# Kernel optimization log

Hardware: AMD Instinct MI355X
Metric: run time of the kernel (lower is better)

## Reference

```python
import jax, jax.numpy as jnp
import numpy as np

B, L, D, H = 4, 2048, 1024, 16
HD = D // H  # head dim = 64


def setup_inputs() -> dict:
    key = jax.random.key(0)
    ks = jax.random.split(key, 8)
    std_qkv = np.sqrt(D + D // H).astype(np.float32)  # matches nn.init.normal_ std in source
    xav = np.sqrt(2.0 / (D + D)).astype(np.float32)   # xavier_normal_ for fc_out
    return {
        "query": jax.random.normal(ks[0], (B, L, D), dtype=jnp.float32),
        "key": jax.random.normal(ks[1], (B, L, D), dtype=jnp.float32),
        "value": jax.random.normal(ks[2], (B, L, D), dtype=jnp.float32),
        "Wq": jax.random.normal(ks[3], (D, D), dtype=jnp.float32) * std_qkv,
        "Wk": jax.random.normal(ks[4], (D, D), dtype=jnp.float32) * std_qkv,
        "Wv": jax.random.normal(ks[5], (D, D), dtype=jnp.float32) * std_qkv,
        "Wo": jax.random.normal(ks[6], (D, D), dtype=jnp.float32) * xav,
        "bo": jnp.zeros((D,), dtype=jnp.float32),
    }


def reference(query, key, value, Wq, Wk, Wv, Wo, bo):
    # Linear projections (torch Linear: x @ W.T), then split heads: b l (h k) -> b h l k
    def split_heads(x):
        b, l, _ = x.shape
        return x.reshape(b, l, H, HD).transpose(0, 2, 1, 3)

    q = split_heads(query @ Wq.T)   # [B,H,L,HD]
    k = split_heads(key @ Wk.T)     # [B,H,T,HD]
    v = split_heads(value @ Wv.T)   # [B,H,T,HD]

    scale = 1.0 / np.sqrt(HD).astype(np.float32)
    energy = jnp.einsum("bhlk,bhtk->bhlt", q, k) * scale  # [B,H,L,T]
    attention = jax.nn.softmax(energy, axis=3)
    out = jnp.einsum("bhlt,bhtv->bhlv", attention, v)     # [B,H,L,HD]
    # b h l v -> b l (h v)
    out = out.transpose(0, 2, 1, 3).reshape(B, L, D)
    out = out @ Wo.T + bo  # dropout_rate=0.0 -> identity
    return out, attention
```

## Files before the change

kernel.cpp:

```cpp
#include <hip/hip_runtime.h>
#include <math.h>

#define Bb 4
#define Ls 2048
#define Dd 1024
#define Hh 16
#define HDm 64
#define ML (Bb*Ls)

typedef double f64x4 __attribute__((ext_vector_type(4)));
typedef float  f32x4 __attribute__((ext_vector_type(4)));
typedef short  bf16x8 __attribute__((ext_vector_type(8)));
typedef unsigned int u32;
typedef unsigned short u16;

__device__ __forceinline__ void gload16(const void* g, void* l) {
  __builtin_amdgcn_global_load_lds(
      (const __attribute__((address_space(1))) u32*)g,
      (__attribute__((address_space(3))) u32*)l, 16, 0, 0);
}

__device__ __forceinline__ u16 f2bf(float f) {
  u32 u = __float_as_uint(f);
  u += 0x7FFFu + ((u >> 16) & 1u);
  return (u16)(u >> 16);
}

__global__ __launch_bounds__(256) void f32_to_bf16(
    const float* __restrict__ in, u16* __restrict__ out, int n8) {
  int i = blockIdx.x * 256 + threadIdx.x;
  if (i >= n8) return;
  const float4* p = (const float4*)(in + (size_t)i * 8);
  float4 a = p[0], c = p[1];
  union { u16 h[8]; uint4 v; } o;
  o.h[0] = f2bf(a.x); o.h[1] = f2bf(a.y); o.h[2] = f2bf(a.z); o.h[3] = f2bf(a.w);
  o.h[4] = f2bf(c.x); o.h[5] = f2bf(c.y); o.h[6] = f2bf(c.z); o.h[7] = f2bf(c.w);
  *(uint4*)(out + (size_t)i * 8) = o.v;
}

__device__ __forceinline__ void gemm_core_nt(
    const float* __restrict__ A, const float* __restrict__ B,
    int bm, int bn, int w, int lrow, int lk, f64x4 acc[4]) {
  const int K = Dd;
  __shared__ __align__(16) float As[2][64 * 16];
  __shared__ __align__(16) float Bs[2][64 * 16];
  const int tid = threadIdx.x;
  const int r = tid >> 2, blk = tid & 3;
  const int sblk = blk ^ ((r >> 1) & 3);
  const int sxw = ((lrow >> 1) & 3) << 2;
  const float* ga = A + (size_t)(bm + r) * K + 4 * sblk;
  const float* gb = B + (size_t)(bn + r) * K + 4 * sblk;

#pragma unroll
  for (int j = 0; j < 4; j++) acc[j] = (f64x4){0., 0., 0., 0.};

  char* la0 = (char*)&As[0][0] + w * 1024;
  char* lb0 = (char*)&Bs[0][0] + w * 1024;
  char* la1 = (char*)&As[1][0] + w * 1024;
  char* lb1 = (char*)&Bs[1][0] + w * 1024;

  gload16(ga, la0);
  gload16(gb, lb0);
  __syncthreads();

  int cur = 0;
  for (int k0 = 16; k0 <= K; k0 += 16) {
    if (k0 < K) {
      gload16(ga + k0, cur ? la0 : la1);
      gload16(gb + k0, cur ? lb0 : lb1);
    }
    const float* Abuf = &As[cur][0];
    const float* Bbuf = &Bs[cur][0];
#pragma unroll
    for (int t = 0; t < 4; t++) {
      double a = (double)Abuf[(16 * w + lrow) * 16 + ((4 * t + lk) ^ sxw)];
#pragma unroll
      for (int j = 0; j < 4; j++) {
        double bv = (double)Bbuf[(16 * j + lrow) * 16 + ((4 * t + lk) ^ sxw)];
        acc[j] = __builtin_amdgcn_mfma_f64_16x16x4f64(a, bv, acc[j], 0, 0, 0);
      }
    }
    __syncthreads();
    cur ^= 1;
  }
}

__global__ __launch_bounds__(256) void gemm_nt_mfma_f64(
    const float* __restrict__ A, const float* __restrict__ B,
    double* __restrict__ C, double outscale) {
  const int tid = threadIdx.x;
  const int lane = tid & 63;
  const int w = tid >> 6;
  const int lrow = lane & 15, lk = lane >> 4;
  const int bm = blockIdx.y * 64, bn = blockIdx.x * 64;
  f64x4 acc[4];
  gemm_core_nt(A, B, bm, bn, w, lrow, lk, acc);
#pragma unroll
  for (int j = 0; j < 4; j++)
#pragma unroll
    for (int d = 0; d < 4; d++) {
      size_t m = (size_t)(bm + 16 * w + 4 * d + lk);
      C[m * Dd + bn + 16 * j + lrow] = acc[j][d] * outscale;
    }
}

__global__ __launch_bounds__(256) void gemm_nt_bf16(
    const u16* __restrict__ A, const u16* __restrict__ B,
    const float* __restrict__ bias, u16* __restrict__ Cb,
    float* __restrict__ Cf) {
  const int K = Dd;
  __shared__ __align__(16) u16 Asb[2][64 * 32];
  __shared__ __align__(16) u16 Bsb[2][64 * 32];
  const int tid = threadIdx.x;
  const int lane = tid & 63;
  const int w = tid >> 6;
  const int lrow = lane & 15, lk = lane >> 4;
  const int bm = blockIdx.y * 64, bn = blockIdx.x * 64;

  const int srow = 16 * w + (lane >> 2);
  const u16* ga = A + (size_t)(bm + srow) * K + 8 * (lane & 3);
  const u16* gb = B + (size_t)(bn + srow) * K + 8 * (lane & 3);
  char* la0 = (char*)&Asb[0][0] + w * 1024;
  char* lb0 = (char*)&Bsb[0][0] + w * 1024;
  char* la1 = (char*)&Asb[1][0] + w * 1024;
  char* lb1 = (char*)&Bsb[1][0] + w * 1024;

  f32x4 acc[4] = {{0.f,0.f,0.f,0.f},{0.f,0.f,0.f,0.f},
                  {0.f,0.f,0.f,0.f},{0.f,0.f,0.f,0.f}};

  gload16(ga, la0);
  gload16(gb, lb0);
  __syncthreads();

  int cur = 0;
  for (int k0 = 32; k0 <= K; k0 += 32) {
    if (k0 < K) {
      gload16(ga + k0, cur ? la0 : la1);
      gload16(gb + k0, cur ? lb0 : lb1);
    }
    const u16* Ab = &Asb[cur][0];
    const u16* Bt = &Bsb[cur][0];
    bf16x8 afr = *(const bf16x8*)&Ab[(16 * w + lrow) * 32 + 8 * lk];
#pragma unroll
    for (int j = 0; j < 4; j++) {
      bf16x8 bfr = *(const bf16x8*)&Bt[(16 * j + lrow) * 32 + 8 * lk];
      acc[j] = __builtin_amdgcn_mfma_f32_16x16x32_bf16(afr, bfr, acc[j], 0, 0, 0);
    }
    __syncthreads();
    cur ^= 1;
  }

#pragma unroll
  for (int j = 0; j < 4; j++)
#pragma unroll
    for (int r = 0; r < 4; r++) {
      size_t m = (size_t)(bm + 16 * w + 4 * lk + r);
      int n = bn + 16 * j + lrow;
      float v = acc[j][r];
      if (bias) v += bias[n];
      if (Cf) Cf[m * Dd + n] = v;
      else    Cb[m * Dd + n] = f2bf(v);
    }
}

__global__ __launch_bounds__(256) void attn_flash(
    double* __restrict__ Qd, const double* __restrict__ Kd,
    const u16* __restrict__ Vf, float* __restrict__ attn,
    u16* __restrict__ O) {
  __shared__ __align__(16) double Kbuf[2][32 * 64];
  __shared__ __align__(16) u16    Vb16[2][32 * 64];
  __shared__ __align__(16) u16    Pb[4][16 * 32];
  __shared__ __align__(16) float  Fs[4][16];

  const int tid = threadIdx.x;
  const int lane = tid & 63;
  const int w = tid >> 6;
  const int lrow = lane & 15;
  const int lk = lane >> 4;
  const int blk = blockIdx.x;
  const int qt = blk & 31;
  const int h = (blk >> 5) & 15;
  const int b = blk >> 9;
  const int l0 = qt * 64;

  const double* Qg = Qd + ((size_t)(b * Ls + l0)) * Dd + h * HDm;
  const double* Kg = Kd + ((size_t)b * Ls) * Dd + h * HDm;
  const u16*    Vg = Vf + ((size_t)b * Ls) * Dd + h * HDm;
  float* aout = attn + ((size_t)((b * Hh + h) * Ls + l0)) * Ls;

  double qreg[16];
#pragma unroll
  for (int t = 0; t < 16; t++)
    qreg[t] = Qg[(size_t)(16 * w + lrow) * Dd + 4 * t + lk];

  const int l16 = (lane & 31) * 16;
  const int halfk = lane >> 5;
  const int sx = (lrow & 7) << 1;

  auto stage = [&](int kts, int bsel) {
#pragma unroll
    for (int jj = 0; jj < 4; jj++) {
      int i = w + 4 * jj;
      int row = 2 * i + halfk;
      int inner = l16 ^ ((row & 7) << 4);
      const char* g = (const char*)Kg + (((size_t)(kts * 32 + row)) << 13) + inner;
      gload16(g, (char*)(&Kbuf[bsel][0]) + i * 1024);
    }
    {
      const char* g = (const char*)Vg +
          ((size_t)(kts * 32 + 8 * w + (lane >> 3))) * (Dd * 2) + (lane & 7) * 16;
      gload16(g, (char*)(&Vb16[bsel][0]) + w * 1024);
    }
  };

  float mreff[4];
  double sacc[4];
  f32x4 pacc[4];
#pragma unroll
  for (int d = 0; d < 4; d++) {
    mreff[d] = -INFINITY;
    sacc[d] = 0.0;
    pacc[d] = (f32x4){0.f, 0.f, 0.f, 0.f};
  }

  stage(0, 0);
  __syncthreads();

  int cur = 0;
  for (int kt = 0; kt < 64; kt++) {
    if (kt < 63) stage(kt + 1, cur ^ 1);

    const double* Kb = &Kbuf[cur][0];

    f64x4 acc0 = {0.0, 0.0, 0.0, 0.0};
    f64x4 acc1 = {0.0, 0.0, 0.0, 0.0};
#pragma unroll
    for (int t = 0; t < 16; t++) {
      int ko = (4 * t + lk) ^ sx;
      double b0 = Kb[lrow * 64 + ko];
      double b1 = Kb[(16 + lrow) * 64 + ko];
      acc0 = __builtin_amdgcn_mfma_f64_16x16x4f64(qreg[t], b0, acc0, 0, 0, 0);
      acc1 = __builtin_amdgcn_mfma_f64_16x16x4f64(qreg[t], b1, acc1, 0, 0, 0);
    }

#pragma unroll
    for (int d = 0; d < 4; d++) {
      double e0 = acc0[d];
      double e1 = acc1[d];
      float tmf = fmaxf((float)e0, (float)e1);
#pragma unroll
      for (int m = 1; m < 16; m <<= 1) tmf = fmaxf(tmf, __shfl_xor(tmf, m));
      float mo_f = mreff[d];
      float ref_f = fmaxf(mo_f, tmf);
      double ref = (double)ref_f;
      float p0 = expf((float)(e0 - ref));
      float p1 = expf((float)(e1 - ref));
      double ts = (double)p0 + (double)p1;
#pragma unroll
      for (int m = 1; m < 16; m <<= 1) ts += __shfl_xor(ts, m);
      float factor = expf(mo_f - ref_f);
      sacc[d] = sacc[d] * (double)factor + ts;
      mreff[d] = ref_f;
      int row = 16 * w + 4 * d + lk;
      aout[(size_t)row * Ls + kt * 32 + lrow] = p0;
      aout[(size_t)row * Ls + kt * 32 + 16 + lrow] = p1;
      if (lrow == 0) {
        ((float*)(Qd + ((size_t)(b * Ls + l0 + row)) * Dd + h * HDm))[kt] = ref_f;
        Fs[w][4 * d + lk] = factor;
      }
      Pb[w][(4 * d + lk) * 32 + lrow] = f2bf(p0);
      Pb[w][(4 * d + lk) * 32 + 16 + lrow] = f2bf(p1);
    }

    bf16x8 afr = *(const bf16x8*)&Pb[w][lrow * 32 + 8 * lk];
    f32x4 fv = *(const f32x4*)&Fs[w][4 * lk];
    const u16* Vb = &Vb16[cur][0];
#pragma unroll
    for (int q = 0; q < 4; q++) {
      pacc[q][0] *= fv[0];
      pacc[q][1] *= fv[1];
      pacc[q][2] *= fv[2];
      pacc[q][3] *= fv[3];
      bf16x8 bfr;
#pragma unroll
      for (int r = 0; r < 8; r++)
        bfr[r] = (short)Vb[(8 * lk + r) * 64 + 16 * q + lrow];
      pacc[q] = __builtin_amdgcn_mfma_f32_16x16x32_bf16(afr, bfr, pacc[q], 0, 0, 0);
    }

    __syncthreads();
    cur ^= 1;
  }

  if (lrow == 0) {
#pragma unroll
    for (int d = 0; d < 4; d++) Fs[w][4 * d + lk] = (float)(1.0 / sacc[d]);
  }
  f32x4 sv = *(const f32x4*)&Fs[w][4 * lk];
#pragma unroll
  for (int q = 0; q < 4; q++)
#pragma unroll
    for (int r = 0; r < 4; r++) {
      int row = 16 * w + 4 * lk + r;
      O[((size_t)(b * Ls + l0 + row)) * Dd + h * HDm + 16 * q + lrow] =
          f2bf(pacc[q][r] * sv[r]);
    }
  if (lrow == 0) {
#pragma unroll
    for (int d = 0; d < 4; d++) {
      int row = 16 * w + 4 * d + lk;
      float* mrow = (float*)(Qd + ((size_t)(b * Ls + l0 + row)) * Dd + h * HDm);
      mrow[64] = mreff[d];
      *(double*)(mrow + 66) = sacc[d];
    }
  }
}

__global__ __launch_bounds__(256) void attn_scale(
    float* __restrict__ attn, const double* __restrict__ Qd) {
  int R = blockIdx.x;
  int b = R >> 15;
  int rem = R & 32767;
  int h = rem >> 11;
  int l = rem & 2047;
  const float* mrow = (const float*)(Qd + ((size_t)(b * Ls + l)) * Dd + h * HDm);
  int tid = threadIdx.x;
  int kt = tid >> 2;
  double mt = (double)mrow[kt];
  double mf = (double)mrow[64];
  double s = *(const double*)(mrow + 66);
  float sc = (float)(exp(mt - mf) / s);
  float4* ap = (float4*)(attn + (size_t)R * Ls + tid * 8);
  float4 a0 = ap[0], a1 = ap[1];
  a0.x *= sc; a0.y *= sc; a0.z *= sc; a0.w *= sc;
  a1.x *= sc; a1.y *= sc; a1.z *= sc; a1.w *= sc;
  ap[0] = a0; ap[1] = a1;
}

extern "C" void kernel_launch(void* const* d_in, const int* in_sizes, int n_in,
                              void* d_out, int out_size, void* d_ws, size_t ws_size,
                              hipStream_t stream) {
  const float* query = (const float*)d_in[0];
  const float* key   = (const float*)d_in[1];
  const float* value = (const float*)d_in[2];
  const float* Wq    = (const float*)d_in[3];
  const float* Wk    = (const float*)d_in[4];
  const float* Wv    = (const float*)d_in[5];
  const float* Wo    = (const float*)d_in[6];
  const float* bo    = (const float*)d_in[7];

  float* out0 = (float*)d_out;
  float* attn = out0 + (size_t)ML * Dd;

  char* ws = (char*)d_ws;
  double* Qd   = (double*)ws;
  double* Kd   = (double*)(ws + (size_t)ML * Dd * 8);
  u16*    Vfb  = (u16*)(ws + (size_t)ML * Dd * 16);
  u16*    Ofb  = (u16*)(ws + (size_t)ML * Dd * 16 + (size_t)ML * Dd * 2);
  u16*    valb = (u16*)(ws + (size_t)ML * Dd * 16 + (size_t)ML * Dd * 4);
  u16*    Wvb  = (u16*)(ws + (size_t)ML * Dd * 16 + (size_t)ML * Dd * 6);
  u16*    Wob  = (u16*)(ws + (size_t)ML * Dd * 16 + (size_t)ML * Dd * 6
                           + (size_t)Dd * Dd * 2);

  dim3 gemm_grid(Dd / 64, ML / 64);

  f32_to_bf16<<<(ML * Dd / 8) / 256, 256, 0, stream>>>(value, valb, ML * Dd / 8);
  f32_to_bf16<<<(Dd * Dd / 8) / 256, 256, 0, stream>>>(Wv, Wvb, Dd * Dd / 8);
  f32_to_bf16<<<(Dd * Dd / 8) / 256, 256, 0, stream>>>(Wo, Wob, Dd * Dd / 8);

  gemm_nt_mfma_f64<<<gemm_grid, 256, 0, stream>>>(query, Wq, Qd, 0.125);
  gemm_nt_mfma_f64<<<gemm_grid, 256, 0, stream>>>(key,   Wk, Kd, 1.0);

  gemm_nt_bf16<<<gemm_grid, 256, 0, stream>>>(valb, Wvb, nullptr, Vfb, nullptr);

  attn_flash<<<Bb * Hh * (Ls / 64), 256, 0, stream>>>(Qd, Kd, Vfb, attn, Ofb);
  attn_scale<<<Bb * Hh * Ls, 256, 0, stream>>>(attn, Qd);

  gemm_nt_bf16<<<gemm_grid, 256, 0, stream>>>(Ofb, Wob, bo, nullptr, out0);
}
```

Baseline: 3.459 ms.

## Emulate FP64 Q/K projections with bf16 limb-split MFMA (Ozaki-style)

Replaces the FP64 MFMA GEMMs for the Q and K projections with an integer-limb decomposition. Inputs and weights are scaled to fixed point and split into five 7-bit limbs stored as bf16. Limb products are then accumulated with bf16 MFMAs into f32 accumulators grouped by limb order, and recombined in double. The goal is to use the much higher bf16 matrix throughput instead of the slow f64 MFMA path, at the cost of extra limb-extraction passes, more launches, and a fixed-point scaling that may truncate precision or overflow for other input ranges.

```diff
diff --git a/kernel.cpp b/kernel.cpp
--- a/kernel.cpp
+++ b/kernel.cpp
@@ -38,69 +38,113 @@
   *(uint4*)(out + (size_t)i * 8) = o.v;
 }
 
-__device__ __forceinline__ void gemm_core_nt(
-    const float* __restrict__ A, const float* __restrict__ B,
-    int bm, int bn, int w, int lrow, int lk, f64x4 acc[4]) {
-  const int K = Dd;
-  __shared__ __align__(16) float As[2][64 * 16];
-  __shared__ __align__(16) float Bs[2][64 * 16];
-  const int tid = threadIdx.x;
-  const int r = tid >> 2, blk = tid & 3;
-  const int sblk = blk ^ ((r >> 1) & 3);
-  const int sxw = ((lrow >> 1) & 3) << 2;
-  const float* ga = A + (size_t)(bm + r) * K + 4 * sblk;
-  const float* gb = B + (size_t)(bn + r) * K + 4 * sblk;
-
-#pragma unroll
-  for (int j = 0; j < 4; j++) acc[j] = (f64x4){0., 0., 0., 0.};
-
-  char* la0 = (char*)&As[0][0] + w * 1024;
-  char* lb0 = (char*)&Bs[0][0] + w * 1024;
-  char* la1 = (char*)&As[1][0] + w * 1024;
-  char* lb1 = (char*)&Bs[1][0] + w * 1024;
-
-  gload16(ga, la0);
-  gload16(gb, lb0);
-  __syncthreads();
-
-  int cur = 0;
-  for (int k0 = 16; k0 <= K; k0 += 16) {
-    if (k0 < K) {
-      gload16(ga + k0, cur ? la0 : la1);
-      gload16(gb + k0, cur ? lb0 : lb1);
-    }
-    const float* Abuf = &As[cur][0];
-    const float* Bbuf = &Bs[cur][0];
-#pragma unroll
-    for (int t = 0; t < 4; t++) {
-      double a = (double)Abuf[(16 * w + lrow) * 16 + ((4 * t + lk) ^ sxw)];
-#pragma unroll
-      for (int j = 0; j < 4; j++) {
-        double bv = (double)Bbuf[(16 * j + lrow) * 16 + ((4 * t + lk) ^ sxw)];
-        acc[j] = __builtin_amdgcn_mfma_f64_16x16x4f64(a, bv, acc[j], 0, 0, 0);
-      }
-    }
-    __syncthreads();
-    cur ^= 1;
-  }
-}
-
-__global__ __launch_bounds__(256) void gemm_nt_mfma_f64(
-    const float* __restrict__ A, const float* __restrict__ B,
-    double* __restrict__ C, double outscale) {
+__global__ __launch_bounds__(256) void extract_limbs(
+    const float* __restrict__ src, u16* __restrict__ dst,
+    size_t planeStride, double scale, int n) {
+  int i = blockIdx.x * 256 + threadIdx.x;
+  if (i >= n) return;
+  long long v = (long long)rint((double)src[i] * scale);
+#pragma unroll
+  for (int p = 0; p < 5; p++) {
+    int li = (int)(((v + 64) & 127) - 64);
+    v = (v - li) >> 7;
+    dst[planeStride * p + i] = f2bf((float)li);
+  }
+}
+
+__global__ __launch_bounds__(256) void gemm_nt_limb(
+    const u16* __restrict__ AL, const u16* __restrict__ WL,
+    double* __restrict__ C, int aPlaneElems, double oscale) {
+  __shared__ __align__(16) u16 lbuf[2][15360];
   const int tid = threadIdx.x;
   const int lane = tid & 63;
   const int w = tid >> 6;
+  const int wr = w >> 1, wc = w & 1;
   const int lrow = lane & 15, lk = lane >> 4;
-  const int bm = blockIdx.y * 64, bn = blockIdx.x * 64;
-  f64x4 acc[4];
-  gemm_core_nt(A, B, bm, bn, w, lrow, lk, acc);
-#pragma unroll
-  for (int j = 0; j < 4; j++)
-#pragma unroll
-    for (int d = 0; d < 4; d++) {
-      size_t m = (size_t)(bm + 16 * w + 4 * d + lk);
-      C[m * Dd + bn + 16 * j + lrow] = acc[j][d] * outscale;
+  const int slk = lk ^ ((lrow >> 1) & 3);
+  const int bm = blockIdx.y * 32, bn = blockIdx.x * 64;
+
+  const u16* gp[8];
+#pragma unroll
+  for (int t = 0; t < 8; t++) {
+    int c = w + 4 * t;
+    if (c < 30) {
+      if (c < 10) {
+        int p = c >> 1;
+        int row = ((c & 1) << 4) + (lane >> 2);
+        int g = (lane & 3) ^ ((row >> 1) & 3);
+        gp[t] = AL + (size_t)p * aPlaneElems + (size_t)(bm + row) * 1024 + g * 8;
+      } else {
+        int cb = c - 10;
+        int p = cb >> 2;
+        int row = ((cb & 3) << 4) + (lane >> 2);
+        int g = (lane & 3) ^ ((row >> 1) & 3);
+        gp[t] = WL + (size_t)p * (1024 * 1024) + (size_t)(bn + row) * 1024 + g * 8;
+      }
+    }
+  }
+
+  f32x4 acc[7][2];
+#pragma unroll
+  for (int b = 0; b < 7; b++)
+#pragma unroll
+    for (int q = 0; q < 2; q++) acc[b][q] = (f32x4){0.f, 0.f, 0.f, 0.f};
+
+#pragma unroll
+  for (int t = 0; t < 8; t++) {
+    int c = w + 4 * t;
+    if (c < 30) gload16(gp[t], (char*)&lbuf[0][0] + c * 1024);
+  }
+  __syncthreads();
+
+  const int abyte = (16 * wr + lrow) * 64 + slk * 16;
+  const int bbyte0 = 10240 + (32 * wc + lrow) * 64 + slk * 16;
+  const int bbyte1 = 10240 + (32 * wc + 16 + lrow) * 64 + slk * 16;
+
+  int cur = 0;
+  for (int step = 0; step < 32; step++) {
+    if (step < 31) {
+#pragma unroll
+      for (int t = 0; t < 8; t++) {
+        int c = w + 4 * t;
+        if (c < 30) {
+          gp[t] += 32;
+          gload16(gp[t], (char*)&lbuf[cur ^ 1][0] + c * 1024);
+        }
+      }
+    }
+    const char* bb = (const char*)&lbuf[cur][0];
+    bf16x8 af[5];
+#pragma unroll
+    for (int i = 0; i < 5; i++)
+      af[i] = *(const bf16x8*)(bb + i * 2048 + abyte);
+#pragma unroll
+    for (int j = 0; j < 5; j++) {
+      bf16x8 b0 = *(const bf16x8*)(bb + j * 4096 + bbyte0);
+      bf16x8 b1 = *(const bf16x8*)(bb + j * 4096 + bbyte1);
+#pragma unroll
+      for (int i = 0; i < 5; i++) {
+        if (i + j >= 2) {
+          acc[i + j - 2][0] = __builtin_amdgcn_mfma_f32_16x16x32_bf16(
+              af[i], b0, acc[i + j - 2][0], 0, 0, 0);
+          acc[i + j - 2][1] = __builtin_amdgcn_mfma_f32_16x16x32_bf16(
+              af[i], b1, acc[i + j - 2][1], 0, 0, 0);
+        }
+      }
+    }
+    __syncthreads();
+    cur ^= 1;
+  }
+
+#pragma unroll
+  for (int q = 0; q < 2; q++)
+#pragma unroll
+    for (int r = 0; r < 4; r++) {
+      double t = (double)acc[6][q][r];
+#pragma unroll
+      for (int b = 5; b >= 0; b--) t = t * 128.0 + (double)acc[b][q][r];
+      size_t m = (size_t)(bm + 16 * wr + 4 * lk + r);
+      C[m * 1024 + bn + 32 * wc + 16 * q + lrow] = t * oscale;
     }
 }
 
@@ -354,24 +398,41 @@
 
   char* ws = (char*)d_ws;
   double* Qd   = (double*)ws;
-  double* Kd   = (double*)(ws + (size_t)ML * Dd * 8);
-  u16*    Vfb  = (u16*)(ws + (size_t)ML * Dd * 16);
-  u16*    Ofb  = (u16*)(ws + (size_t)ML * Dd * 16 + (size_t)ML * Dd * 2);
-  u16*    valb = (u16*)(ws + (size_t)ML * Dd * 16 + (size_t)ML * Dd * 4);
-  u16*    Wvb  = (u16*)(ws + (size_t)ML * Dd * 16 + (size_t)ML * Dd * 6);
-  u16*    Wob  = (u16*)(ws + (size_t)ML * Dd * 16 + (size_t)ML * Dd * 6
-                           + (size_t)Dd * Dd * 2);
+  double* Kd   = (double*)(ws + 67108864ull);
+  u16*    Vfb  = (u16*)(ws + 134217728ull);
+  u16*    Ofb  = (u16*)(ws + 150994944ull);
+  u16*    valb = (u16*)(ws + 167772160ull);
+  u16*    Wvb  = (u16*)(ws + 184549376ull);
+  u16*    Wob  = (u16*)(ws + 186646528ull);
+  u16*    LW   = (u16*)(ws + 188743680ull);
+  u16*    LA   = (u16*)(ws + 199229440ull);
+
+  const int halfElems = (ML / 2) * Dd;
+  const int wElems = Dd * Dd;
+  const double SA = 268435456.0;
+  const double SW = 8388608.0;
+  const double OSQ = 0.125 / 137438953472.0;
+  const double OSK = 1.0 / 137438953472.0;
 
   dim3 gemm_grid(Dd / 64, ML / 64);
+  dim3 limb_grid(Dd / 64, (ML / 2) / 32);
 
   f32_to_bf16<<<(ML * Dd / 8) / 256, 256, 0, stream>>>(value, valb, ML * Dd / 8);
   f32_to_bf16<<<(Dd * Dd / 8) / 256, 256, 0, stream>>>(Wv, Wvb, Dd * Dd / 8);
   f32_to_bf16<<<(Dd * Dd / 8) / 256, 256, 0, stream>>>(Wo, Wob, Dd * Dd / 8);
-
-  gemm_nt_mfma_f64<<<gemm_grid, 256, 0, stream>>>(query, Wq, Qd, 0.125);
-  gemm_nt_mfma_f64<<<gemm_grid, 256, 0, stream>>>(key,   Wk, Kd, 1.0);
-
   gemm_nt_bf16<<<gemm_grid, 256, 0, stream>>>(valb, Wvb, nullptr, Vfb, nullptr);
+
+  extract_limbs<<<wElems / 256, 256, 0, stream>>>(Wq, LW, (size_t)wElems, SW, wElems);
+  extract_limbs<<<halfElems / 256, 256, 0, stream>>>(query, LA, (size_t)halfElems, SA, halfElems);
+  gemm_nt_limb<<<limb_grid, 256, 0, stream>>>(LA, LW, Qd, halfElems, OSQ);
+  extract_limbs<<<halfElems / 256, 256, 0, stream>>>(query + (size_t)halfElems, LA, (size_t)halfElems, SA, halfElems);
+  gemm_nt_limb<<<limb_grid, 256, 0, stream>>>(LA, LW, Qd + (size_t)halfElems, halfElems, OSQ);
+
+  extract_limbs<<<wElems / 256, 256, 0, stream>>>(Wk, LW, (size_t)wElems, SW, wElems);
+  extract_limbs<<<halfElems / 256, 256, 0, stream>>>(key, LA, (size_t)halfElems, SA, halfElems);
+  gemm_nt_limb<<<limb_grid, 256, 0, stream>>>(LA, LW, Kd, halfElems, OSK);
+  extract_limbs<<<halfElems / 256, 256, 0, stream>>>(key + (size_t)halfElems, LA, (size_t)halfElems, SA, halfElems);
+  gemm_nt_limb<<<limb_grid, 256, 0, stream>>>(LA, LW, Kd + (size_t)halfElems, halfElems, OSK);
 
   attn_flash<<<Bb * Hh * (Ls / 64), 256, 0, stream>>>(Qd, Kd, Vfb, attn, Ofb);
   attn_scale<<<Bb * Hh * Ls, 256, 0, stream>>>(attn, Qd);
```

Result: no change. 3.501 ms (+1.2%).
